# Performance work log

Hardware: AMD Instinct MI355X
Metric: run time of the kernel (lower is better)

Reference implementation:

```python
import jax, jax.numpy as jnp
import numpy as np

B, A, L, D, IN = 4096, 11, 8, 256, 4
HID = 64  # mlp_dim in MS_HGNN modules
LINE = 64  # line_embedding output dim


def setup_inputs() -> dict:
    key = jax.random.key(0)
    ks = jax.random.split(key, 17)
    s = 0.02
    f = jnp.float32
    return {
        "inputs": jax.random.normal(ks[0], (B * A, L, IN), f),
        "W_in": jax.random.normal(ks[1], (IN, D), f) * s,
        "b_in": jnp.zeros((D,), f),
        "W_pos": jax.random.normal(ks[2], (2 * D, D), f) * s,
        "b_pos": jnp.zeros((D,), f),
        "W_fc2": jax.random.normal(ks[3], (L * D, D), f) * s,
        "b_fc2": jnp.zeros((D,), f),
        "W_fc3": jax.random.normal(ks[4], (D + A, D), f) * s,
        "b_fc3": jnp.zeros((D,), f),
        "Wh1": jax.random.normal(ks[5], (D, HID), f) * s,
        "We1": jax.random.normal(ks[6], (2 * HID, HID), f) * s,
        "Wn1": jax.random.normal(ks[7], (HID, D), f) * s,
        "Wh2": jax.random.normal(ks[8], (D, HID), f) * s,
        "We2": jax.random.normal(ks[9], (2 * HID, HID), f) * s,
        "Wn2": jax.random.normal(ks[10], (HID, D), f) * s,
        "W_line": jax.random.normal(ks[11], (D, LINE), f) * s,
        "batch_size": B,
        "agent_num": A,
    }


def _nmp(xf, Wh, We, Wn, w=None):
    # one round of neural message passing over the (hyper)graph of agents
    h = jax.nn.relu(xf @ Wh)  # [B, A, HID]
    b, a, hd = h.shape
    hi = jnp.broadcast_to(h[:, :, None, :], (b, a, a, hd))
    hj = jnp.broadcast_to(h[:, None, :, :], (b, a, a, hd))
    e = jax.nn.relu(jnp.concatenate([hi, hj], -1) @ We)  # [B, A, A, HID]
    if w is None:
        agg = e.mean(axis=2)
    else:
        agg = (w[..., None] * e).sum(axis=2) / (w.sum(axis=2)[..., None] + 1e-6)
    return agg @ Wn  # [B, A, D]


def reference(inputs, W_in, b_in, W_pos, b_pos, W_fc2, b_fc2, W_fc3, b_fc3,
              Wh1, We1, Wn1, Wh2, We2, Wn2, W_line, batch_size, agent_num):
    d = W_in.shape[1]
    length = inputs.shape[1]
    # input_fc
    tf_in = inputs @ W_in + b_in  # [B*A, L, D]
    # positional encoding (sin/cos interleaved), concat + fc (dropout in eval)
    pos = jnp.arange(length, dtype=tf_in.dtype)[:, None]
    div = jnp.exp(jnp.arange(0, d, 2, dtype=tf_in.dtype) * (-np.log(10000.0) / d))
    ang = pos * div  # [L, D/2]
    pe = jnp.stack([jnp.sin(ang), jnp.cos(ang)], -1).reshape(length, d)
    x = jnp.concatenate([tf_in, jnp.broadcast_to(pe, tf_in.shape)], -1) @ W_pos + b_pos
    # flatten time, input_fc2
    x = x.reshape(batch_size, agent_num, length * d)
    ftraj = x @ W_fc2 + b_fc2  # [B, A, D]
    # add_category (identity one-hot per agent) + input_fc3
    eye = jnp.broadcast_to(jnp.eye(agent_num, dtype=ftraj.dtype),
                           (batch_size, agent_num, agent_num))
    ftraj = jnp.concatenate([ftraj, eye], -1) @ W_fc3 + b_fc3
    # cosine-similarity correlation + per-scene adaptive thresholding
    q = ftraj / jnp.linalg.norm(ftraj, axis=2, keepdims=True)
    corr = jnp.einsum('bad,bcd->bac', q, q)
    a = corr.min(axis=(1, 2), keepdims=True)
    thr = jnp.where(a < 0.4, 0.4,
                    jnp.where((a > 0.4) & (a < 0.6), a + 0.1, a + 0.03))
    corr = jnp.where(corr < thr, jnp.zeros_like(corr), corr)
    adj = (corr > 0).astype(ftraj.dtype)  # binarized dynamic grouping mask
    # ordinary fully-connected interaction
    ftraj_inter = _nmp(ftraj, Wh1, We1, Wn1)
    # group-masked hyper interaction + line embedding
    hyp = _nmp(ftraj, Wh2, We2, Wn2, adj)
    feat_one = hyp @ W_line  # [B, A, LINE]
    out = jnp.concatenate([ftraj, ftraj_inter, feat_one], -1)
    return out.reshape(batch_size * agent_num, -1)
```

## Files before the change

### kernel.cpp

```cpp
#include <hip/hip_runtime.h>

#define TPB 256

constexpr int B_ = 4096, A_ = 11;
constexpr int R_ = B_ * A_;
constexpr int K32 = 32;

constexpr int M_O     = 0;
constexpr int M2_O    = 8192;
constexpr int WC_O    = 16384;
constexpr int XBASE_O = 17408;
constexpr int PE_O    = 17664;
constexpr int XB_O    = 19712;
constexpr int CB_O    = 21760;
constexpr int B2_O    = 22016;
constexpr int WN2L_O  = 24832;
constexpr int MH1_O   = 28928;
constexpr int BH1_O   = 30976;
constexpr int MH2_O   = 16384;
constexpr int BH2_O   = 18432;
constexpr int U1_O    = 32768;
constexpr int SZ_RH   = R_ * 64;
constexpr int V1_O    = U1_O + SZ_RH;
constexpr int U2_O    = V1_O + SZ_RH;
constexpr int V2_O    = U2_O + SZ_RH;


__global__ __launch_bounds__(TPB) void k_preA(const float* __restrict__ Win,
                                              const float* __restrict__ bin,
                                              const float* __restrict__ Wpos,
                                              const float* __restrict__ bpos,
                                              float* __restrict__ ws) {
    __shared__ float red[8 * 33];
    const int t = threadIdx.x, o8 = t & 31, ks = t >> 5;
    const int bx = blockIdx.x;
    if (bx < 32) {
        int o = bx * 32 + o8, i = o >> 8, j = o & 255;
        const float* Ar = Win + i * 256;
        float p = 0.f;
        #pragma unroll 8
        for (int d = ks * 32; d < ks * 32 + 32; ++d) p += Ar[d] * Wpos[d * 256 + j];
        red[ks * 33 + o8] = p;
        __syncthreads();
        if (t < 32) {
            float s = 0.f;
            #pragma unroll
            for (int m = 0; m < 8; ++m) s += red[m * 33 + t];
            ws[WC_O + bx * 32 + t] = s;
        }
    } else if (bx < 40) {
        int j = (bx - 32) * 32 + o8;
        float p = 0.f;
        #pragma unroll 8
        for (int d = ks * 32; d < ks * 32 + 32; ++d) p += bin[d] * Wpos[d * 256 + j];
        red[ks * 33 + o8] = p;
        __syncthreads();
        if (t < 32) {
            float s = bpos[(bx - 32) * 32 + t];
            #pragma unroll
            for (int m = 0; m < 8; ++m) s += red[m * 33 + t];
            ws[XBASE_O + (bx - 32) * 32 + t] = s;
        }
    } else {
        int o = (bx - 40) * 256 + t;
        int l = o >> 8, dd = o & 255;
        const float c0 = -logf(10000.f) / 256.f;
        float freq = expf((float)(dd & ~1) * c0);
        float ang = (float)l * freq;
        ws[PE_O + o] = (dd & 1) ? cosf(ang) : sinf(ang);
    }
}

__global__ __launch_bounds__(TPB) void k_preB(const float* __restrict__ Wpos,
                                              float* __restrict__ ws) {
    __shared__ float red[8 * 33];
    const int t = threadIdx.x, o8 = t & 31, ks = t >> 5;
    int o = blockIdx.x * 32 + o8, l = o >> 8, j = o & 255;
    const float* per = ws + PE_O + l * 256;
    float p = 0.f;
    #pragma unroll 8
    for (int d = ks * 32; d < ks * 32 + 32; ++d) p += per[d] * Wpos[(256 + d) * 256 + j];
    red[ks * 33 + o8] = p;
    __syncthreads();
    if (t < 32) {
        int oo = blockIdx.x * 32 + t;
        float s = ws[XBASE_O + (oo & 255)];
        #pragma unroll
        for (int m = 0; m < 8; ++m) s += red[m * 33 + t];
        ws[XB_O + oo] = s;
    }
}

__global__ __launch_bounds__(TPB) void k_preC(const float* __restrict__ Wfc2,
                                              const float* __restrict__ bfc2,
                                              float* __restrict__ ws) {
    __shared__ float red[8 * 33];
    const int t = threadIdx.x, o8 = t & 31, ks = t >> 5;
    const int bx = blockIdx.x;
    if (bx < 256) {
        int o = bx * 32 + o8, k = o >> 8, j = o & 255;
        int l = k >> 2, i = k & 3;
        const float* Ar = ws + WC_O + i * 256;
        const float* Br = Wfc2 + l * 65536 + j;
        float p = 0.f;
        #pragma unroll 8
        for (int d = ks * 32; d < ks * 32 + 32; ++d) p += Ar[d] * Br[d * 256];
        red[ks * 33 + o8] = p;
        __syncthreads();
        if (t < 32) {
            float s = 0.f;
            #pragma unroll
            for (int m = 0; m < 8; ++m) s += red[m * 33 + t];
            ws[M_O + bx * 32 + t] = s;
        }
    } else {
        int j = (bx - 256) * 32 + o8;
        const float* Ar = ws + XB_O;
        float p = 0.f;
        #pragma unroll 4
        for (int dk = ks * 256; dk < ks * 256 + 256; ++dk) p += Ar[dk] * Wfc2[dk * 256 + j];
        red[ks * 33 + o8] = p;
        __syncthreads();
        if (t < 32) {
            int jj = (bx - 256) * 32 + t;
            float s = bfc2[jj];
            #pragma unroll
            for (int m = 0; m < 8; ++m) s += red[m * 33 + t];
            ws[CB_O + jj] = s;
        }
    }
}

__global__ __launch_bounds__(TPB) void k_preD(const float* __restrict__ Wfc3,
                                              const float* __restrict__ bfc3,
                                              const float* __restrict__ Wn2,
                                              const float* __restrict__ Wline,
                                              float* __restrict__ ws) {
    __shared__ float red[8 * 33];
    const int t = threadIdx.x, o8 = t & 31, ks = t >> 5;
    const int bx = blockIdx.x;
    if (bx < 256) {
        int o = bx * 32 + o8, k = o >> 8, j = o & 255;
        const float* Ar = ws + M_O + k * 256;
        float p = 0.f;
        #pragma unroll 8
        for (int d = ks * 32; d < ks * 32 + 32; ++d) p += Ar[d] * Wfc3[d * 256 + j];
        red[ks * 33 + o8] = p;
        __syncthreads();
        if (t < 32) {
            float s = 0.f;
            #pragma unroll
            for (int m = 0; m < 8; ++m) s += red[m * 33 + t];
            ws[M2_O + bx * 32 + t] = s;
        }
    } else if (bx < 344) {
        int o = (bx - 256) * 32 + o8, a = o >> 8, j = o & 255;
        const float* Ar = ws + CB_O;
        float p = 0.f;
        #pragma unroll 8
        for (int d = ks * 32; d < ks * 32 + 32; ++d) p += Ar[d] * Wfc3[d * 256 + j];
        red[ks * 33 + o8] = p;
        __syncthreads();
        if (t < 32) {
            int oo = (bx - 256) * 32 + t;
            int aa = oo >> 8, jj = oo & 255;
            float s = bfc3[jj] + Wfc3[(256 + aa) * 256 + jj];
            #pragma unroll
            for (int m = 0; m < 8; ++m) s += red[m * 33 + t];
            ws[B2_O + oo] = s;
        }
    } else {
        int o = (bx - 344) * 32 + o8, k = o >> 6, c = o & 63;
        const float* Ar = Wn2 + k * 256;
        float p = 0.f;
        #pragma unroll 8
        for (int d = ks * 32; d < ks * 32 + 32; ++d) p += Ar[d] * Wline[d * 64 + c];
        red[ks * 33 + o8] = p;
        __syncthreads();
        if (t < 32) {
            float s = 0.f;
            #pragma unroll
            for (int m = 0; m < 8; ++m) s += red[m * 33 + t];
            ws[WN2L_O + (bx - 344) * 32 + t] = s;
        }
    }
}

__global__ __launch_bounds__(TPB) void k_preE(const float* __restrict__ Wh1,
                                              const float* __restrict__ Wh2,
                                              float* __restrict__ ws) {
    __shared__ float red[8 * 33];
    const int t = threadIdx.x, o8 = t & 31, ks = t >> 5;
    const int bx = blockIdx.x;
    const float* Aw;  const float* Bw;  int oo_base;  int out_o;  int mode;
    if (bx < 64)       { mode = 0; out_o = MH1_O; oo_base = bx * 32;         Bw = Wh1; }
    else if (bx < 86)  { mode = 1; out_o = BH1_O; oo_base = (bx - 64) * 32;  Bw = Wh1; }
    else if (bx < 150) { mode = 0; out_o = MH2_O; oo_base = (bx - 86) * 32;  Bw = Wh2; }
    else               { mode = 1; out_o = BH2_O; oo_base = (bx - 150) * 32; Bw = Wh2; }
    int o = oo_base + o8;
    int r = o >> 6, c = o & 63;
    Aw = ws + (mode == 0 ? M2_O : B2_O) + r * 256;
    float p = 0.f;
    #pragma unroll 8
    for (int d = ks * 32; d < ks * 32 + 32; ++d) p += Aw[d] * Bw[d * 64 + c];
    red[ks * 33 + o8] = p;
    __syncthreads();
    if (t < 32) {
        float s = 0.f;
        #pragma unroll
        for (int m = 0; m < 8; ++m) s += red[m * 33 + t];
        ws[out_o + oo_base + t] = s;
    }
}


__global__ __launch_bounds__(TPB) void k_rows3(const float* __restrict__ in,
                                               const float* __restrict__ We1g,
                                               const float* __restrict__ We2g,
                                               float* __restrict__ ws,
                                               float* __restrict__ out) {
    __shared__ float inS[64 * 32];
    __shared__ float hS[64 * 64];
    __shared__ float Bs[4096];
    const int t = threadIdx.x;
    const int rowBase = blockIdx.x * 64;
    const int tg = t >> 4, tc = t & 15;
    const int r0 = tg * 4;

    {
        const float4* src = (const float4*)(in + (size_t)rowBase * K32);
        float4* dst = (float4*)inS;
        dst[t] = src[t];
        dst[t + 256] = src[t + 256];
    }
    __syncthreads();

    int ag[4];
    #pragma unroll
    for (int r = 0; r < 4; ++r) ag[r] = (rowBase + r0 + r) % 11;

    {
        float acc[4][16];
        #pragma unroll
        for (int r = 0; r < 4; ++r)
            #pragma unroll
            for (int c = 0; c < 16; ++c) acc[r][c] = 0.f;
        for (int kh = 0; kh < 2; ++kh) {
            if (kh) __syncthreads();
            {
                const float4* src = (const float4*)(ws + M2_O + kh * 4096);
                float4* dst = (float4*)Bs;
                #pragma unroll
                for (int m = 0; m < 4; ++m) dst[t + m * 256] = src[t + m * 256];
            }
            __syncthreads();
            #pragma unroll
            for (int kq = 0; kq < 4; ++kq) {
                float avq[4][4];
                #pragma unroll
                for (int r = 0; r < 4; ++r) {
                    float4 a4 = *(const float4*)&inS[(r0 + r) * 32 + kh * 16 + kq * 4];
                    avq[r][0] = a4.x; avq[r][1] = a4.y; avq[r][2] = a4.z; avq[r][3] = a4.w;
                }
                #pragma unroll
                for (int kk = 0; kk < 4; ++kk) {
                    float4 b[4];
                    #pragma unroll
                    for (int j = 0; j < 4; ++j)
                        b[j] = *(const float4*)&Bs[(kq * 4 + kk) * 256 + tc * 16 + j * 4];
                    #pragma unroll
                    for (int r = 0; r < 4; ++r) {
                        float a = avq[r][kk];
                        #pragma unroll
                        for (int j = 0; j < 4; ++j) {
                            acc[r][j * 4 + 0] += a * b[j].x;
                            acc[r][j * 4 + 1] += a * b[j].y;
                            acc[r][j * 4 + 2] += a * b[j].z;
                            acc[r][j * 4 + 3] += a * b[j].w;
                        }
                    }
                }
            }
        }
        #pragma unroll
        for (int r = 0; r < 4; ++r) {
            size_t ob = (size_t)(rowBase + r0 + r) * 576 + tc * 16;
            const float* bb = ws + B2_O + ag[r] * 256 + tc * 16;
            #pragma unroll
            for (int j = 0; j < 4; ++j) {
                float4 b = *(const float4*)&bb[j * 4];
                *(float4*)&out[ob + j * 4] =
                    make_float4(acc[r][j * 4 + 0] + b.x, acc[r][j * 4 + 1] + b.y,
                                acc[r][j * 4 + 2] + b.z, acc[r][j * 4 + 3] + b.w);
            }
        }
    }

    const int c0 = tc * 4;
    for (int s = 0; s < 2; ++s) {
        const int mh_o = s ? MH2_O : MH1_O;
        const int bh_o = s ? BH2_O : BH1_O;
        const float* We = s ? We2g : We1g;
        float* ug = ws + (s ? U2_O : U1_O);
        float* vg = ws + (s ? V2_O : V1_O);

        __syncthreads();
        {
            const float4* src = (const float4*)(ws + mh_o);
            float4* dst = (float4*)Bs;
            dst[t] = src[t];
            if (t < 256) dst[t + 256] = src[t + 256];
        }
        __syncthreads();
        float hacc[4][4];
        #pragma unroll
        for (int r = 0; r < 4; ++r)
            #pragma unroll
            for (int c = 0; c < 4; ++c) hacc[r][c] = 0.f;
        #pragma unroll
        for (int kq = 0; kq < 8; ++kq) {
            float avq[4][4];
            #pragma unroll
            for (int r = 0; r < 4; ++r) {
                float4 a4 = *(const float4*)&inS[(r0 + r) * 32 + kq * 4];
                avq[r][0] = a4.x; avq[r][1] = a4.y; avq[r][2] = a4.z; avq[r][3] = a4.w;
            }
            #pragma unroll
            for (int kk = 0; kk < 4; ++kk) {
                float4 b = *(const float4*)&Bs[(kq * 4 + kk) * 64 + c0];
                #pragma unroll
                for (int r = 0; r < 4; ++r) {
                    float a = avq[r][kk];
                    hacc[r][0] += a * b.x; hacc[r][1] += a * b.y;
                    hacc[r][2] += a * b.z; hacc[r][3] += a * b.w;
                }
            }
        }
        #pragma unroll
        for (int r = 0; r < 4; ++r) {
            float4 b = *(const float4*)&ws[bh_o + ag[r] * 64 + c0];
            float4 h = make_float4(fmaxf(hacc[r][0] + b.x, 0.f), fmaxf(hacc[r][1] + b.y, 0.f),
                                   fmaxf(hacc[r][2] + b.z, 0.f), fmaxf(hacc[r][3] + b.w, 0.f));
            *(float4*)&hS[(r0 + r) * 64 + c0] = h;
        }
        __syncthreads();

        float ua[4][4], va[4][4];
        #pragma unroll
        for (int r = 0; r < 4; ++r)
            #pragma unroll
            for (int c = 0; c < 4; ++c) { ua[r][c] = 0.f; va[r][c] = 0.f; }
        for (int kh = 0; kh < 2; ++kh) {
            if (kh) __syncthreads();
            {
                const float4* s0 = (const float4*)(We + kh * 2048);
                const float4* s1 = (const float4*)(We + 4096 + kh * 2048);
                float4* dst = (float4*)Bs;
                dst[t] = s0[t];
                if (t < 256) dst[t + 256] = s0[t + 256];
                dst[t + 512] = s1[t];
                if (t < 256) dst[t + 768] = s1[t + 256];
            }
            __syncthreads();
            #pragma unroll
            for (int kq = 0; kq < 8; ++kq) {
                float avq[4][4];
                #pragma unroll
                for (int r = 0; r < 4; ++r) {
                    float4 a4 = *(const float4*)&hS[(r0 + r) * 64 + kh * 32 + kq * 4];
                    avq[r][0] = a4.x; avq[r][1] = a4.y; avq[r][2] = a4.z; avq[r][3] = a4.w;
                }
                #pragma unroll
                for (int kk = 0; kk < 4; ++kk) {
                    float4 bu = *(const float4*)&Bs[(kq * 4 + kk) * 64 + c0];
                    float4 bv = *(const float4*)&Bs[2048 + (kq * 4 + kk) * 64 + c0];
                    #pragma unroll
                    for (int r = 0; r < 4; ++r) {
                        float a = avq[r][kk];
                        ua[r][0] += a * bu.x; ua[r][1] += a * bu.y;
                        ua[r][2] += a * bu.z; ua[r][3] += a * bu.w;
                        va[r][0] += a * bv.x; va[r][1] += a * bv.y;
                        va[r][2] += a * bv.z; va[r][3] += a * bv.w;
                    }
                }
            }
        }
        #pragma unroll
        for (int r = 0; r < 4; ++r) {
            size_t rb = (size_t)(rowBase + r0 + r) * 64 + c0;
            *(float4*)&ug[rb] = make_float4(ua[r][0], ua[r][1], ua[r][2], ua[r][3]);
            *(float4*)&vg[rb] = make_float4(va[r][0], va[r][1], va[r][2], va[r][3]);
        }
    }
}


__global__ __launch_bounds__(TPB) void k_scene3(const float* __restrict__ out_ft,
                                                const float* __restrict__ Wn1,
                                                float* __restrict__ ws,
                                                float* __restrict__ out) {
    __shared__ float ftS[11 * 260];
    __shared__ float u1s[704], v1s[704], u2s[704], v2s[704];
    __shared__ float dots[121];
    __shared__ float corrv[121];
    __shared__ float red[4];
    __shared__ float sthr;
    const int t = threadIdx.x;
    const int scene = blockIdx.x;
    const int base = scene * 11;

    for (int o = t; o < 704; o += TPB) {
        int row = o >> 6, c4 = o & 63;
        ((float4*)ftS)[row * 65 + c4] =
            *(const float4*)&out_ft[(size_t)(base + row) * 576 + c4 * 4];
    }
    {
        const float4* su1 = (const float4*)(ws + U1_O + (size_t)base * 64);
        const float4* sv1 = (const float4*)(ws + V1_O + (size_t)base * 64);
        const float4* su2 = (const float4*)(ws + U2_O + (size_t)base * 64);
        const float4* sv2 = (const float4*)(ws + V2_O + (size_t)base * 64);
        if (t < 176) {
            ((float4*)u1s)[t] = su1[t];
            ((float4*)v1s)[t] = sv1[t];
            ((float4*)u2s)[t] = su2[t];
            ((float4*)v2s)[t] = sv2[t];
        }
    }
    __syncthreads();

    if (t < 121) {
        int i = t / 11, j = t - i * 11;
        float s = 0.f;
        #pragma unroll 8
        for (int kq = 0; kq < 64; ++kq) {
            float4 a = *(const float4*)&ftS[i * 260 + kq * 4];
            float4 b = *(const float4*)&ftS[j * 260 + kq * 4];
            s += a.x * b.x + a.y * b.y + a.z * b.z + a.w * b.w;
        }
        dots[t] = s;
    }
    __syncthreads();
    if (t < 121) {
        int i = t / 11, j = t - i * 11;
        corrv[t] = dots[t] * rsqrtf(dots[i * 11 + i] * dots[j * 11 + j]);
    }
    __syncthreads();
    float v = (t < 121) ? corrv[t] : 3.0e38f;
    for (int off = 32; off > 0; off >>= 1) v = fminf(v, __shfl_down(v, off));
    if ((t & 63) == 0) red[t >> 6] = v;
    __syncthreads();
    if (t == 0) {
        float a = fminf(fminf(red[0], red[1]), fminf(red[2], red[3]));
        sthr = (a < 0.4f) ? 0.4f : ((a > 0.4f && a < 0.6f) ? a + 0.1f : a + 0.03f);
    }
    __syncthreads();
    const float thr = sthr;

    {
        const int c = t & 63, g = t >> 6;
        const int nr = (g == 3) ? 2 : 3;
        float u1[3], u2[3], s1[3], s2[3], cnt[3];
        #pragma unroll
        for (int r = 0; r < 3; ++r) { s1[r] = 0.f; s2[r] = 0.f; cnt[r] = 0.f; }
        for (int r = 0; r < nr; ++r) {
            u1[r] = u1s[(g + 4 * r) * 64 + c];
            u2[r] = u2s[(g + 4 * r) * 64 + c];
        }
        #pragma unroll
        for (int j = 0; j < 11; ++j) {
            float vv1 = v1s[j * 64 + c];
            float vv2 = v2s[j * 64 + c];
            for (int r = 0; r < nr; ++r) {
                float cw = corrv[(g + 4 * r) * 11 + j];
                s1[r] += fmaxf(u1[r] + vv1, 0.f);
                float adj = (cw >= thr) ? 1.f : 0.f;
                s2[r] += adj * fmaxf(u2[r] + vv2, 0.f);
                cnt[r] += adj;
            }
        }
        for (int r = 0; r < nr; ++r) {
            u1s[(g + 4 * r) * 64 + c] = s1[r] * (1.f / 11.f);
            u2s[(g + 4 * r) * 64 + c] = s2[r] / (cnt[r] + 1e-6f);
        }
    }
    __syncthreads();

    {
        const int c = t;
        float breg[64];
        #pragma unroll
        for (int k = 0; k < 64; ++k) breg[k] = Wn1[k * 256 + c];
        float acc[11];
        #pragma unroll
        for (int i = 0; i < 11; ++i) acc[i] = 0.f;
        #pragma unroll
        for (int kq = 0; kq < 16; ++kq) {
            #pragma unroll
            for (int i = 0; i < 11; ++i) {
                float4 a = *(const float4*)&u1s[i * 64 + kq * 4];
                acc[i] += a.x * breg[kq * 4 + 0] + a.y * breg[kq * 4 + 1]
                        + a.z * breg[kq * 4 + 2] + a.w * breg[kq * 4 + 3];
            }
        }
        #pragma unroll
        for (int i = 0; i < 11; ++i)
            out[(size_t)(base + i) * 576 + 256 + c] = acc[i];
    }
    {
        const int c = t & 63, g = t >> 6;
        const int nr = (g == 3) ? 2 : 3;
        float wreg[64];
        #pragma unroll
        for (int k = 0; k < 64; ++k) wreg[k] = ws[WN2L_O + k * 64 + c];
        float acc[3] = {0.f, 0.f, 0.f};
        #pragma unroll
        for (int kq = 0; kq < 16; ++kq) {
            for (int r = 0; r < nr; ++r) {
                float4 a = *(const float4*)&u2s[(g + 4 * r) * 64 + kq * 4];
                acc[r] += a.x * wreg[kq * 4 + 0] + a.y * wreg[kq * 4 + 1]
                        + a.z * wreg[kq * 4 + 2] + a.w * wreg[kq * 4 + 3];
            }
        }
        for (int r = 0; r < nr; ++r)
            out[(size_t)(base + g + 4 * r) * 576 + 512 + c] = acc[r];
    }
}

extern "C" void kernel_launch(void* const* d_in, const int* in_sizes, int n_in,
                              void* d_out, int out_size, void* d_ws, size_t ws_size,
                              hipStream_t stream) {
    (void)in_sizes; (void)n_in; (void)out_size; (void)ws_size;
    const float* in     = (const float*)d_in[0];
    const float* W_in   = (const float*)d_in[1];
    const float* b_in   = (const float*)d_in[2];
    const float* W_pos  = (const float*)d_in[3];
    const float* b_pos  = (const float*)d_in[4];
    const float* W_fc2  = (const float*)d_in[5];
    const float* b_fc2  = (const float*)d_in[6];
    const float* W_fc3  = (const float*)d_in[7];
    const float* b_fc3  = (const float*)d_in[8];
    const float* Wh1    = (const float*)d_in[9];
    const float* We1    = (const float*)d_in[10];
    const float* Wn1    = (const float*)d_in[11];
    const float* Wh2    = (const float*)d_in[12];
    const float* We2    = (const float*)d_in[13];
    const float* Wn2    = (const float*)d_in[14];
    const float* W_line = (const float*)d_in[15];
    float* out = (float*)d_out;
    float* ws  = (float*)d_ws;

    k_preA<<<48, TPB, 0, stream>>>(W_in, b_in, W_pos, b_pos, ws);
    k_preB<<<64, TPB, 0, stream>>>(W_pos, ws);
    k_preC<<<264, TPB, 0, stream>>>(W_fc2, b_fc2, ws);
    k_preD<<<472, TPB, 0, stream>>>(W_fc3, b_fc3, Wn2, W_line, ws);
    k_preE<<<172, TPB, 0, stream>>>(Wh1, Wh2, ws);
    k_rows3<<<R_ / 64, TPB, 0, stream>>>(in, We1, We2, ws, out);
    k_scene3<<<B_, TPB, 0, stream>>>(out, Wn1, ws, out);
}
```

Measured before the change: 177.6 us.

## Fuse per-row projection and per-scene message passing into one kernel

Replaces the separate row kernel (which wrote u/v intermediates to workspace) and the scene kernel (which reread ftraj and u/v) with a single kernel. Each 64-lane wave handles one whole scene and computes ftraj, the correlation threshold, both message-passing rounds and the output projections on-chip. The positional-encoding precompute is also merged into one setup kernel, and the Wn2·W_line product moves there, cutting one launch. This removes the large intermediate global round-trips and a launch. The cost is heavy register use (11-row accumulators) and many block barriers in the fused kernel.

```diff
diff --git a/kernel.cpp b/kernel.cpp
--- a/kernel.cpp
+++ b/kernel.cpp
@@ -4,13 +4,10 @@
 
 constexpr int B_ = 4096, A_ = 11;
 constexpr int R_ = B_ * A_;
-constexpr int K32 = 32;
 
 constexpr int M_O     = 0;
 constexpr int M2_O    = 8192;
 constexpr int WC_O    = 16384;
-constexpr int XBASE_O = 17408;
-constexpr int PE_O    = 17664;
 constexpr int XB_O    = 19712;
 constexpr int CB_O    = 21760;
 constexpr int B2_O    = 22016;
@@ -19,18 +16,15 @@
 constexpr int BH1_O   = 30976;
 constexpr int MH2_O   = 16384;
 constexpr int BH2_O   = 18432;
-constexpr int U1_O    = 32768;
-constexpr int SZ_RH   = R_ * 64;
-constexpr int V1_O    = U1_O + SZ_RH;
-constexpr int U2_O    = V1_O + SZ_RH;
-constexpr int V2_O    = U2_O + SZ_RH;
-
-
-__global__ __launch_bounds__(TPB) void k_preA(const float* __restrict__ Win,
-                                              const float* __restrict__ bin,
-                                              const float* __restrict__ Wpos,
-                                              const float* __restrict__ bpos,
-                                              float* __restrict__ ws) {
+
+
+__global__ __launch_bounds__(TPB) void k_preAB(const float* __restrict__ Win,
+                                               const float* __restrict__ bin,
+                                               const float* __restrict__ Wpos,
+                                               const float* __restrict__ bpos,
+                                               const float* __restrict__ Wn2,
+                                               const float* __restrict__ Wline,
+                                               float* __restrict__ ws) {
     __shared__ float red[8 * 33];
     const int t = threadIdx.x, o8 = t & 31, ks = t >> 5;
     const int bx = blockIdx.x;
@@ -48,46 +42,44 @@
             for (int m = 0; m < 8; ++m) s += red[m * 33 + t];
             ws[WC_O + bx * 32 + t] = s;
         }
-    } else if (bx < 40) {
-        int j = (bx - 32) * 32 + o8;
+    } else if (bx < 96) {
+        int o = (bx - 32) * 32 + o8, l = o >> 8, j = o & 255;
+        const float c0 = -logf(10000.f) / 256.f;
+        float p = 0.f;
+        for (int d = ks * 64; d < ks * 64 + 64; ++d) {
+            float a;
+            if (d < 256) a = bin[d];
+            else {
+                int dd = d - 256;
+                float freq = expf((float)(dd & ~1) * c0);
+                float ang = (float)l * freq;
+                a = (dd & 1) ? cosf(ang) : sinf(ang);
+            }
+            p += a * Wpos[d * 256 + j];
+        }
+        red[ks * 33 + o8] = p;
+        __syncthreads();
+        if (t < 32) {
+            int oo = (bx - 32) * 32 + t;
+            float s = bpos[oo & 255];
+            #pragma unroll
+            for (int m = 0; m < 8; ++m) s += red[m * 33 + t];
+            ws[XB_O + oo] = s;
+        }
+    } else {
+        int o = (bx - 96) * 32 + o8, k = o >> 6, c = o & 63;
+        const float* Ar = Wn2 + k * 256;
         float p = 0.f;
         #pragma unroll 8
-        for (int d = ks * 32; d < ks * 32 + 32; ++d) p += bin[d] * Wpos[d * 256 + j];
-        red[ks * 33 + o8] = p;
-        __syncthreads();
-        if (t < 32) {
-            float s = bpos[(bx - 32) * 32 + t];
-            #pragma unroll
-            for (int m = 0; m < 8; ++m) s += red[m * 33 + t];
-            ws[XBASE_O + (bx - 32) * 32 + t] = s;
-        }
-    } else {
-        int o = (bx - 40) * 256 + t;
-        int l = o >> 8, dd = o & 255;
-        const float c0 = -logf(10000.f) / 256.f;
-        float freq = expf((float)(dd & ~1) * c0);
-        float ang = (float)l * freq;
-        ws[PE_O + o] = (dd & 1) ? cosf(ang) : sinf(ang);
-    }
-}
-
-__global__ __launch_bounds__(TPB) void k_preB(const float* __restrict__ Wpos,
-                                              float* __restrict__ ws) {
-    __shared__ float red[8 * 33];
-    const int t = threadIdx.x, o8 = t & 31, ks = t >> 5;
-    int o = blockIdx.x * 32 + o8, l = o >> 8, j = o & 255;
-    const float* per = ws + PE_O + l * 256;
-    float p = 0.f;
-    #pragma unroll 8
-    for (int d = ks * 32; d < ks * 32 + 32; ++d) p += per[d] * Wpos[(256 + d) * 256 + j];
-    red[ks * 33 + o8] = p;
-    __syncthreads();
-    if (t < 32) {
-        int oo = blockIdx.x * 32 + t;
-        float s = ws[XBASE_O + (oo & 255)];
-        #pragma unroll
-        for (int m = 0; m < 8; ++m) s += red[m * 33 + t];
-        ws[XB_O + oo] = s;
+        for (int d = ks * 32; d < ks * 32 + 32; ++d) p += Ar[d] * Wline[d * 64 + c];
+        red[ks * 33 + o8] = p;
+        __syncthreads();
+        if (t < 32) {
+            float s = 0.f;
+            #pragma unroll
+            for (int m = 0; m < 8; ++m) s += red[m * 33 + t];
+            ws[WN2L_O + (bx - 96) * 32 + t] = s;
+        }
     }
 }
 
@@ -133,8 +125,6 @@
 
 __global__ __launch_bounds__(TPB) void k_preD(const float* __restrict__ Wfc3,
                                               const float* __restrict__ bfc3,
-                                              const float* __restrict__ Wn2,
-                                              const float* __restrict__ Wline,
                                               float* __restrict__ ws) {
     __shared__ float red[8 * 33];
     const int t = threadIdx.x, o8 = t & 31, ks = t >> 5;
@@ -153,8 +143,8 @@
             for (int m = 0; m < 8; ++m) s += red[m * 33 + t];
             ws[M2_O + bx * 32 + t] = s;
         }
-    } else if (bx < 344) {
-        int o = (bx - 256) * 32 + o8, a = o >> 8, j = o & 255;
+    } else {
+        int o = (bx - 256) * 32 + o8, j = o & 255;
         const float* Ar = ws + CB_O;
         float p = 0.f;
         #pragma unroll 8
@@ -168,20 +158,6 @@
             #pragma unroll
             for (int m = 0; m < 8; ++m) s += red[m * 33 + t];
             ws[B2_O + oo] = s;
-        }
-    } else {
-        int o = (bx - 344) * 32 + o8, k = o >> 6, c = o & 63;
-        const float* Ar = Wn2 + k * 256;
-        float p = 0.f;
-        #pragma unroll 8
-        for (int d = ks * 32; d < ks * 32 + 32; ++d) p += Ar[d] * Wline[d * 64 + c];
-        red[ks * 33 + o8] = p;
-        __syncthreads();
-        if (t < 32) {
-            float s = 0.f;
-            #pragma unroll
-            for (int m = 0; m < 8; ++m) s += red[m * 33 + t];
-            ws[WN2L_O + (bx - 344) * 32 + t] = s;
         }
     }
 }
@@ -192,14 +168,14 @@
     __shared__ float red[8 * 33];
     const int t = threadIdx.x, o8 = t & 31, ks = t >> 5;
     const int bx = blockIdx.x;
-    const float* Aw;  const float* Bw;  int oo_base;  int out_o;  int mode;
+    const float* Bw;  int oo_base;  int out_o;  int mode;
     if (bx < 64)       { mode = 0; out_o = MH1_O; oo_base = bx * 32;         Bw = Wh1; }
     else if (bx < 86)  { mode = 1; out_o = BH1_O; oo_base = (bx - 64) * 32;  Bw = Wh1; }
     else if (bx < 150) { mode = 0; out_o = MH2_O; oo_base = (bx - 86) * 32;  Bw = Wh2; }
     else               { mode = 1; out_o = BH2_O; oo_base = (bx - 150) * 32; Bw = Wh2; }
     int o = oo_base + o8;
     int r = o >> 6, c = o & 63;
-    Aw = ws + (mode == 0 ? M2_O : B2_O) + r * 256;
+    const float* Aw = ws + (mode == 0 ? M2_O : B2_O) + r * 256;
     float p = 0.f;
     #pragma unroll 8
     for (int d = ks * 32; d < ks * 32 + 32; ++d) p += Aw[d] * Bw[d * 64 + c];
@@ -214,315 +190,262 @@
 }
 
 
-__global__ __launch_bounds__(TPB) void k_rows3(const float* __restrict__ in,
-                                               const float* __restrict__ We1g,
-                                               const float* __restrict__ We2g,
-                                               float* __restrict__ ws,
-                                               float* __restrict__ out) {
-    __shared__ float inS[64 * 32];
-    __shared__ float hS[64 * 64];
-    __shared__ float Bs[4096];
+__device__ __forceinline__ void fma4(float4& a, float s, const float4& b) {
+    a.x += s * b.x; a.y += s * b.y; a.z += s * b.z; a.w += s * b.w;
+}
+
+__global__ __launch_bounds__(TPB, 4) void k_fused(const float* __restrict__ in,
+                                                  const float* __restrict__ We1g,
+                                                  const float* __restrict__ We2g,
+                                                  const float* __restrict__ Wn1,
+                                                  const float* __restrict__ ws,
+                                                  float* __restrict__ out) {
+    __shared__ float inS[44 * 36];
+    __shared__ float cS[44 * 68];
+    __shared__ float Bs[2048];
+    __shared__ float dotsS[4 * 121];
+    __shared__ float corrS[4 * 121];
     const int t = threadIdx.x;
-    const int rowBase = blockIdx.x * 64;
-    const int tg = t >> 4, tc = t & 15;
-    const int r0 = tg * 4;
-
+    const int w = t >> 6, lane = t & 63;
+    const int rowBlk = blockIdx.x * 44;
+    const int wr = w * 11;
+
+    for (int o = t; o < 352; o += TPB) {
+        int row = o >> 3, c4 = o & 7;
+        *(float4*)&inS[row * 36 + c4 * 4] =
+            *(const float4*)&in[(size_t)(rowBlk + row) * 32 + c4 * 4];
+    }
+
+    int pi0 = 0, pj0 = 0, pi1 = 0, pj1 = 0;
+    const bool has0 = lane < 66;
+    const bool has1 = lane < 2;
     {
-        const float4* src = (const float4*)(in + (size_t)rowBase * K32);
-        float4* dst = (float4*)inS;
-        dst[t] = src[t];
-        dst[t + 256] = src[t + 256];
-    }
-    __syncthreads();
-
-    int ag[4];
+        int q = has0 ? lane : 0, i = 0;
+        while (q >= 11 - i) { q -= 11 - i; ++i; }
+        pi0 = i; pj0 = i + q;
+        if (has1) {
+            int q2 = lane + 64, i2 = 0;
+            while (q2 >= 11 - i2) { q2 -= 11 - i2; ++i2; }
+            pi1 = i2; pj1 = i2 + q2;
+        }
+    }
+    __syncthreads();
+
+    float4 ft[11];
+    {
+        const float* M2g = ws + M2_O;
+        #pragma unroll
+        for (int i = 0; i < 11; ++i) ft[i] = make_float4(0.f, 0.f, 0.f, 0.f);
+        #pragma unroll
+        for (int kq = 0; kq < 8; ++kq) {
+            float4 b[4];
+            #pragma unroll
+            for (int kk = 0; kk < 4; ++kk)
+                b[kk] = *(const float4*)&M2g[(kq * 4 + kk) * 256 + lane * 4];
+            #pragma unroll
+            for (int i = 0; i < 11; ++i) {
+                float4 a4 = *(const float4*)&inS[(wr + i) * 36 + kq * 4];
+                fma4(ft[i], a4.x, b[0]); fma4(ft[i], a4.y, b[1]);
+                fma4(ft[i], a4.z, b[2]); fma4(ft[i], a4.w, b[3]);
+            }
+        }
+        #pragma unroll
+        for (int i = 0; i < 11; ++i) {
+            float4 b2 = *(const float4*)&ws[B2_O + i * 256 + lane * 4];
+            ft[i].x += b2.x; ft[i].y += b2.y; ft[i].z += b2.z; ft[i].w += b2.w;
+            *(float4*)&out[(size_t)(rowBlk + wr + i) * 576 + lane * 4] = ft[i];
+        }
+    }
+
+    float dacc0 = 0.f, dacc1 = 0.f;
+    for (int ch = 0; ch < 4; ++ch) {
+        __syncthreads();
+        if ((lane >> 4) == ch) {
+            int cl = (lane & 15) * 4;
+            #pragma unroll
+            for (int i = 0; i < 11; ++i)
+                *(float4*)&cS[(wr + i) * 68 + cl] = ft[i];
+        }
+        __syncthreads();
+        if (has0) {
+            const float* ra = &cS[(wr + pi0) * 68];
+            const float* rb = &cS[(wr + pj0) * 68];
+            #pragma unroll
+            for (int cc = 0; cc < 16; ++cc) {
+                float4 a = *(const float4*)&ra[cc * 4];
+                float4 b = *(const float4*)&rb[cc * 4];
+                dacc0 += a.x * b.x + a.y * b.y + a.z * b.z + a.w * b.w;
+            }
+        }
+        if (has1) {
+            const float* ra = &cS[(wr + pi1) * 68];
+            const float* rb = &cS[(wr + pj1) * 68];
+            #pragma unroll
+            for (int cc = 0; cc < 16; ++cc) {
+                float4 a = *(const float4*)&ra[cc * 4];
+                float4 b = *(const float4*)&rb[cc * 4];
+                dacc1 += a.x * b.x + a.y * b.y + a.z * b.z + a.w * b.w;
+            }
+        }
+    }
+    if (has0) { dotsS[w * 121 + pi0 * 11 + pj0] = dacc0;
+                dotsS[w * 121 + pj0 * 11 + pi0] = dacc0; }
+    if (has1) { dotsS[w * 121 + pi1 * 11 + pj1] = dacc1;
+                dotsS[w * 121 + pj1 * 11 + pi1] = dacc1; }
+    __syncthreads();
+
+    float thr;
+    {
+        const float* dw = &dotsS[w * 121];
+        int q = lane, i = q / 11, j = q % 11;
+        float c0 = dw[q] * rsqrtf(dw[i * 11 + i] * dw[j * 11 + j]);
+        corrS[w * 121 + q] = c0;
+        float mn = c0;
+        int q2 = lane + 64;
+        if (q2 < 121) {
+            int i2 = q2 / 11, j2 = q2 % 11;
+            float c1 = dw[q2] * rsqrtf(dw[i2 * 11 + i2] * dw[j2 * 11 + j2]);
+            corrS[w * 121 + q2] = c1;
+            mn = fminf(mn, c1);
+        }
+        #pragma unroll
+        for (int off = 32; off; off >>= 1) mn = fminf(mn, __shfl_xor(mn, off));
+        thr = (mn < 0.4f) ? 0.4f : ((mn > 0.4f && mn < 0.6f) ? mn + 0.1f : mn + 0.03f);
+    }
+
+    float agg1[11], agg2[11];
+    for (int st = 0; st < 2; ++st) {
+        const float* Weg = st ? We2g : We1g;
+        const float* bhg = ws + (st ? BH2_O : BH1_O);
+        __syncthreads();
+        {
+            const float4* src = (const float4*)(ws + (st ? MH2_O : MH1_O));
+            ((float4*)Bs)[t] = src[t];
+            ((float4*)Bs)[t + 256] = src[t + 256];
+        }
+        __syncthreads();
+        float h[11];
+        {
+            #pragma unroll
+            for (int i = 0; i < 11; ++i) h[i] = 0.f;
+            #pragma unroll
+            for (int kq = 0; kq < 8; ++kq) {
+                float bq[4];
+                #pragma unroll
+                for (int kk = 0; kk < 4; ++kk) bq[kk] = Bs[(kq * 4 + kk) * 64 + lane];
+                #pragma unroll
+                for (int i = 0; i < 11; ++i) {
+                    float4 a4 = *(const float4*)&inS[(wr + i) * 36 + kq * 4];
+                    h[i] += a4.x * bq[0] + a4.y * bq[1] + a4.z * bq[2] + a4.w * bq[3];
+                }
+            }
+            #pragma unroll
+            for (int i = 0; i < 11; ++i)
+                h[i] = fmaxf(h[i] + bhg[i * 64 + lane], 0.f);
+        }
+        __syncthreads();
+        #pragma unroll
+        for (int i = 0; i < 11; ++i) cS[(wr + i) * 68 + lane] = h[i];
+
+        float u[11], v[11];
+        #pragma unroll
+        for (int i = 0; i < 11; ++i) { u[i] = 0.f; v[i] = 0.f; }
+        for (int kh = 0; kh < 4; ++kh) {
+            __syncthreads();
+            {
+                int k = t >> 4, c4 = t & 15;
+                ((float4*)Bs)[t] = *(const float4*)&Weg[(kh * 16 + k) * 64 + c4 * 4];
+                ((float4*)(Bs + 1024))[t] = *(const float4*)&Weg[(64 + kh * 16 + k) * 64 + c4 * 4];
+            }
+            __syncthreads();
+            #pragma unroll
+            for (int kq = 0; kq < 4; ++kq) {
+                float bu[4], bv[4];
+                #pragma unroll
+                for (int kk = 0; kk < 4; ++kk) {
+                    bu[kk] = Bs[(kq * 4 + kk) * 64 + lane];
+                    bv[kk] = Bs[1024 + (kq * 4 + kk) * 64 + lane];
+                }
+                #pragma unroll
+                for (int i = 0; i < 11; ++i) {
+                    float4 a4 = *(const float4*)&cS[(wr + i) * 68 + kh * 16 + kq * 4];
+                    u[i] += a4.x * bu[0] + a4.y * bu[1] + a4.z * bu[2] + a4.w * bu[3];
+                    v[i] += a4.x * bv[0] + a4.y * bv[1] + a4.z * bv[2] + a4.w * bv[3];
+                }
+            }
+        }
+        if (st == 0) {
+            #pragma unroll
+            for (int i = 0; i < 11; ++i) {
+                float s = 0.f;
+                #pragma unroll
+                for (int j = 0; j < 11; ++j) s += fmaxf(u[i] + v[j], 0.f);
+                agg1[i] = s * (1.f / 11.f);
+            }
+        } else {
+            #pragma unroll
+            for (int i = 0; i < 11; ++i) {
+                float s = 0.f, cnt = 0.f;
+                #pragma unroll
+                for (int j = 0; j < 11; ++j) {
+                    float adj = (corrS[w * 121 + i * 11 + j] >= thr) ? 1.f : 0.f;
+                    s += adj * fmaxf(u[i] + v[j], 0.f);
+                    cnt += adj;
+                }
+                agg2[i] = s / (cnt + 1e-6f);
+            }
+        }
+    }
+
+    __syncthreads();
     #pragma unroll
-    for (int r = 0; r < 4; ++r) ag[r] = (rowBase + r0 + r) % 11;
-
+    for (int i = 0; i < 11; ++i) cS[(wr + i) * 68 + lane] = agg1[i];
+    __syncthreads();
     {
-        float acc[4][16];
-        #pragma unroll
-        for (int r = 0; r < 4; ++r)
-            #pragma unroll
-            for (int c = 0; c < 16; ++c) acc[r][c] = 0.f;
-        for (int kh = 0; kh < 2; ++kh) {
-            if (kh) __syncthreads();
-            {
-                const float4* src = (const float4*)(ws + M2_O + kh * 4096);
-                float4* dst = (float4*)Bs;
-                #pragma unroll
-                for (int m = 0; m < 4; ++m) dst[t + m * 256] = src[t + m * 256];
-            }
-            __syncthreads();
-            #pragma unroll
-            for (int kq = 0; kq < 4; ++kq) {
-                float avq[4][4];
-                #pragma unroll
-                for (int r = 0; r < 4; ++r) {
-                    float4 a4 = *(const float4*)&inS[(r0 + r) * 32 + kh * 16 + kq * 4];
-                    avq[r][0] = a4.x; avq[r][1] = a4.y; avq[r][2] = a4.z; avq[r][3] = a4.w;
-                }
-                #pragma unroll
-                for (int kk = 0; kk < 4; ++kk) {
-                    float4 b[4];
-                    #pragma unroll
-                    for (int j = 0; j < 4; ++j)
-                        b[j] = *(const float4*)&Bs[(kq * 4 + kk) * 256 + tc * 16 + j * 4];
-                    #pragma unroll
-                    for (int r = 0; r < 4; ++r) {
-                        float a = avq[r][kk];
-                        #pragma unroll
-                        for (int j = 0; j < 4; ++j) {
-                            acc[r][j * 4 + 0] += a * b[j].x;
-                            acc[r][j * 4 + 1] += a * b[j].y;
-                            acc[r][j * 4 + 2] += a * b[j].z;
-                            acc[r][j * 4 + 3] += a * b[j].w;
-                        }
-                    }
-                }
-            }
-        }
-        #pragma unroll
-        for (int r = 0; r < 4; ++r) {
-            size_t ob = (size_t)(rowBase + r0 + r) * 576 + tc * 16;
-            const float* bb = ws + B2_O + ag[r] * 256 + tc * 16;
-            #pragma unroll
-            for (int j = 0; j < 4; ++j) {
-                float4 b = *(const float4*)&bb[j * 4];
-                *(float4*)&out[ob + j * 4] =
-                    make_float4(acc[r][j * 4 + 0] + b.x, acc[r][j * 4 + 1] + b.y,
-                                acc[r][j * 4 + 2] + b.z, acc[r][j * 4 + 3] + b.w);
-            }
-        }
-    }
-
-    const int c0 = tc * 4;
-    for (int s = 0; s < 2; ++s) {
-        const int mh_o = s ? MH2_O : MH1_O;
-        const int bh_o = s ? BH2_O : BH1_O;
-        const float* We = s ? We2g : We1g;
-        float* ug = ws + (s ? U2_O : U1_O);
-        float* vg = ws + (s ? V2_O : V1_O);
-
-        __syncthreads();
-        {
-            const float4* src = (const float4*)(ws + mh_o);
-            float4* dst = (float4*)Bs;
-            dst[t] = src[t];
-            if (t < 256) dst[t + 256] = src[t + 256];
-        }
-        __syncthreads();
-        float hacc[4][4];
-        #pragma unroll
-        for (int r = 0; r < 4; ++r)
-            #pragma unroll
-            for (int c = 0; c < 4; ++c) hacc[r][c] = 0.f;
-        #pragma unroll
-        for (int kq = 0; kq < 8; ++kq) {
-            float avq[4][4];
-            #pragma unroll
-            for (int r = 0; r < 4; ++r) {
-                float4 a4 = *(const float4*)&inS[(r0 + r) * 32 + kq * 4];
-                avq[r][0] = a4.x; avq[r][1] = a4.y; avq[r][2] = a4.z; avq[r][3] = a4.w;
-            }
-            #pragma unroll
-            for (int kk = 0; kk < 4; ++kk) {
-                float4 b = *(const float4*)&Bs[(kq * 4 + kk) * 64 + c0];
-                #pragma unroll
-                for (int r = 0; r < 4; ++r) {
-                    float a = avq[r][kk];
-                    hacc[r][0] += a * b.x; hacc[r][1] += a * b.y;
-                    hacc[r][2] += a * b.z; hacc[r][3] += a * b.w;
-                }
-            }
-        }
-        #pragma unroll
-        for (int r = 0; r < 4; ++r) {
-            float4 b = *(const float4*)&ws[bh_o + ag[r] * 64 + c0];
-            float4 h = make_float4(fmaxf(hacc[r][0] + b.x, 0.f), fmaxf(hacc[r][1] + b.y, 0.f),
-                                   fmaxf(hacc[r][2] + b.z, 0.f), fmaxf(hacc[r][3] + b.w, 0.f));
-            *(float4*)&hS[(r0 + r) * 64 + c0] = h;
-        }
-        __syncthreads();
-
-        float ua[4][4], va[4][4];
-        #pragma unroll
-        for (int r = 0; r < 4; ++r)
-            #pragma unroll
-            for (int c = 0; c < 4; ++c) { ua[r][c] = 0.f; va[r][c] = 0.f; }
-        for (int kh = 0; kh < 2; ++kh) {
-            if (kh) __syncthreads();
-            {
-                const float4* s0 = (const float4*)(We + kh * 2048);
-                const float4* s1 = (const float4*)(We + 4096 + kh * 2048);
-                float4* dst = (float4*)Bs;
-                dst[t] = s0[t];
-                if (t < 256) dst[t + 256] = s0[t + 256];
-                dst[t + 512] = s1[t];
-                if (t < 256) dst[t + 768] = s1[t + 256];
-            }
-            __syncthreads();
-            #pragma unroll
-            for (int kq = 0; kq < 8; ++kq) {
-                float avq[4][4];
-                #pragma unroll
-                for (int r = 0; r < 4; ++r) {
-                    float4 a4 = *(const float4*)&hS[(r0 + r) * 64 + kh * 32 + kq * 4];
-                    avq[r][0] = a4.x; avq[r][1] = a4.y; avq[r][2] = a4.z; avq[r][3] = a4.w;
-                }
-                #pragma unroll
-                for (int kk = 0; kk < 4; ++kk) {
-                    float4 bu = *(const float4*)&Bs[(kq * 4 + kk) * 64 + c0];
-                    float4 bv = *(const float4*)&Bs[2048 + (kq * 4 + kk) * 64 + c0];
-                    #pragma unroll
-                    for (int r = 0; r < 4; ++r) {
-                        float a = avq[r][kk];
-                        ua[r][0] += a * bu.x; ua[r][1] += a * bu.y;
-                        ua[r][2] += a * bu.z; ua[r][3] += a * bu.w;
-                        va[r][0] += a * bv.x; va[r][1] += a * bv.y;
-                        va[r][2] += a * bv.z; va[r][3] += a * bv.w;
-                    }
-                }
-            }
-        }
-        #pragma unroll
-        for (int r = 0; r < 4; ++r) {
-            size_t rb = (size_t)(rowBase + r0 + r) * 64 + c0;
-            *(float4*)&ug[rb] = make_float4(ua[r][0], ua[r][1], ua[r][2], ua[r][3]);
-            *(float4*)&vg[rb] = make_float4(va[r][0], va[r][1], va[r][2], va[r][3]);
-        }
-    }
-}
-
-
-__global__ __launch_bounds__(TPB) void k_scene3(const float* __restrict__ out_ft,
-                                                const float* __restrict__ Wn1,
-                                                float* __restrict__ ws,
-                                                float* __restrict__ out) {
-    __shared__ float ftS[11 * 260];
-    __shared__ float u1s[704], v1s[704], u2s[704], v2s[704];
-    __shared__ float dots[121];
-    __shared__ float corrv[121];
-    __shared__ float red[4];
-    __shared__ float sthr;
-    const int t = threadIdx.x;
-    const int scene = blockIdx.x;
-    const int base = scene * 11;
-
-    for (int o = t; o < 704; o += TPB) {
-        int row = o >> 6, c4 = o & 63;
-        ((float4*)ftS)[row * 65 + c4] =
-            *(const float4*)&out_ft[(size_t)(base + row) * 576 + c4 * 4];
-    }
+        float4 acc[11];
+        #pragma unroll
+        for (int i = 0; i < 11; ++i) acc[i] = make_float4(0.f, 0.f, 0.f, 0.f);
+        #pragma unroll 4
+        for (int kq = 0; kq < 16; ++kq) {
+            float4 b[4];
+            #pragma unroll
+            for (int kk = 0; kk < 4; ++kk)
+                b[kk] = *(const float4*)&Wn1[(kq * 4 + kk) * 256 + lane * 4];
+            #pragma unroll
+            for (int i = 0; i < 11; ++i) {
+                float4 a4 = *(const float4*)&cS[(wr + i) * 68 + kq * 4];
+                fma4(acc[i], a4.x, b[0]); fma4(acc[i], a4.y, b[1]);
+                fma4(acc[i], a4.z, b[2]); fma4(acc[i], a4.w, b[3]);
+            }
+        }
+        #pragma unroll
+        for (int i = 0; i < 11; ++i)
+            *(float4*)&out[(size_t)(rowBlk + wr + i) * 576 + 256 + lane * 4] = acc[i];
+    }
+
+    __syncthreads();
+    #pragma unroll
+    for (int i = 0; i < 11; ++i) cS[(wr + i) * 68 + lane] = agg2[i];
+    __syncthreads();
     {
-        const float4* su1 = (const float4*)(ws + U1_O + (size_t)base * 64);
-        const float4* sv1 = (const float4*)(ws + V1_O + (size_t)base * 64);
-        const float4* su2 = (const float4*)(ws + U2_O + (size_t)base * 64);
-        const float4* sv2 = (const float4*)(ws + V2_O + (size_t)base * 64);
-        if (t < 176) {
-            ((float4*)u1s)[t] = su1[t];
-            ((float4*)v1s)[t] = sv1[t];
-            ((float4*)u2s)[t] = su2[t];
-            ((float4*)v2s)[t] = sv2[t];
-        }
-    }
-    __syncthreads();
-
-    if (t < 121) {
-        int i = t / 11, j = t - i * 11;
-        float s = 0.f;
-        #pragma unroll 8
-        for (int kq = 0; kq < 64; ++kq) {
-            float4 a = *(const float4*)&ftS[i * 260 + kq * 4];
-            float4 b = *(const float4*)&ftS[j * 260 + kq * 4];
-            s += a.x * b.x + a.y * b.y + a.z * b.z + a.w * b.w;
-        }
-        dots[t] = s;
-    }
-    __syncthreads();
-    if (t < 121) {
-        int i = t / 11, j = t - i * 11;
-        corrv[t] = dots[t] * rsqrtf(dots[i * 11 + i] * dots[j * 11 + j]);
-    }
-    __syncthreads();
-    float v = (t < 121) ? corrv[t] : 3.0e38f;
-    for (int off = 32; off > 0; off >>= 1) v = fminf(v, __shfl_down(v, off));
-    if ((t & 63) == 0) red[t >> 6] = v;
-    __syncthreads();
-    if (t == 0) {
-        float a = fminf(fminf(red[0], red[1]), fminf(red[2], red[3]));
-        sthr = (a < 0.4f) ? 0.4f : ((a > 0.4f && a < 0.6f) ? a + 0.1f : a + 0.03f);
-    }
-    __syncthreads();
-    const float thr = sthr;
-
-    {
-        const int c = t & 63, g = t >> 6;
-        const int nr = (g == 3) ? 2 : 3;
-        float u1[3], u2[3], s1[3], s2[3], cnt[3];
-        #pragma unroll
-        for (int r = 0; r < 3; ++r) { s1[r] = 0.f; s2[r] = 0.f; cnt[r] = 0.f; }
-        for (int r = 0; r < nr; ++r) {
-            u1[r] = u1s[(g + 4 * r) * 64 + c];
-            u2[r] = u2s[(g + 4 * r) * 64 + c];
-        }
-        #pragma unroll
-        for (int j = 0; j < 11; ++j) {
-            float vv1 = v1s[j * 64 + c];
-            float vv2 = v2s[j * 64 + c];
-            for (int r = 0; r < nr; ++r) {
-                float cw = corrv[(g + 4 * r) * 11 + j];
-                s1[r] += fmaxf(u1[r] + vv1, 0.f);
-                float adj = (cw >= thr) ? 1.f : 0.f;
-                s2[r] += adj * fmaxf(u2[r] + vv2, 0.f);
-                cnt[r] += adj;
-            }
-        }
-        for (int r = 0; r < nr; ++r) {
-            u1s[(g + 4 * r) * 64 + c] = s1[r] * (1.f / 11.f);
-            u2s[(g + 4 * r) * 64 + c] = s2[r] / (cnt[r] + 1e-6f);
-        }
-    }
-    __syncthreads();
-
-    {
-        const int c = t;
-        float breg[64];
-        #pragma unroll
-        for (int k = 0; k < 64; ++k) breg[k] = Wn1[k * 256 + c];
-        float acc[11];
-        #pragma unroll
-        for (int i = 0; i < 11; ++i) acc[i] = 0.f;
-        #pragma unroll
+        float f[11];
+        #pragma unroll
+        for (int i = 0; i < 11; ++i) f[i] = 0.f;
+        const float* W2 = ws + WN2L_O;
+        #pragma unroll 4
         for (int kq = 0; kq < 16; ++kq) {
+            float bq[4];
+            #pragma unroll
+            for (int kk = 0; kk < 4; ++kk) bq[kk] = W2[(kq * 4 + kk) * 64 + lane];
             #pragma unroll
             for (int i = 0; i < 11; ++i) {
-                float4 a = *(const float4*)&u1s[i * 64 + kq * 4];
-                acc[i] += a.x * breg[kq * 4 + 0] + a.y * breg[kq * 4 + 1]
-                        + a.z * breg[kq * 4 + 2] + a.w * breg[kq * 4 + 3];
+                float4 a4 = *(const float4*)&cS[(wr + i) * 68 + kq * 4];
+                f[i] += a4.x * bq[0] + a4.y * bq[1] + a4.z * bq[2] + a4.w * bq[3];
             }
         }
         #pragma unroll
         for (int i = 0; i < 11; ++i)
-            out[(size_t)(base + i) * 576 + 256 + c] = acc[i];
-    }
-    {
-        const int c = t & 63, g = t >> 6;
-        const int nr = (g == 3) ? 2 : 3;
-        float wreg[64];
-        #pragma unroll
-        for (int k = 0; k < 64; ++k) wreg[k] = ws[WN2L_O + k * 64 + c];
-        float acc[3] = {0.f, 0.f, 0.f};
-        #pragma unroll
-        for (int kq = 0; kq < 16; ++kq) {
-            for (int r = 0; r < nr; ++r) {
-                float4 a = *(const float4*)&u2s[(g + 4 * r) * 64 + kq * 4];
-                acc[r] += a.x * wreg[kq * 4 + 0] + a.y * wreg[kq * 4 + 1]
-                        + a.z * wreg[kq * 4 + 2] + a.w * wreg[kq * 4 + 3];
-            }
-        }
-        for (int r = 0; r < nr; ++r)
-            out[(size_t)(base + g + 4 * r) * 576 + 512 + c] = acc[r];
+            out[(size_t)(rowBlk + wr + i) * 576 + 512 + lane] = f[i];
     }
 }
 
@@ -549,11 +472,9 @@
     float* out = (float*)d_out;
     float* ws  = (float*)d_ws;
 
-    k_preA<<<48, TPB, 0, stream>>>(W_in, b_in, W_pos, b_pos, ws);
-    k_preB<<<64, TPB, 0, stream>>>(W_pos, ws);
+    k_preAB<<<224, TPB, 0, stream>>>(W_in, b_in, W_pos, b_pos, Wn2, W_line, ws);
     k_preC<<<264, TPB, 0, stream>>>(W_fc2, b_fc2, ws);
-    k_preD<<<472, TPB, 0, stream>>>(W_fc3, b_fc3, Wn2, W_line, ws);
+    k_preD<<<344, TPB, 0, stream>>>(W_fc3, b_fc3, ws);
     k_preE<<<172, TPB, 0, stream>>>(Wh1, Wh2, ws);
-    k_rows3<<<R_ / 64, TPB, 0, stream>>>(in, We1, We2, ws, out);
-    k_scene3<<<B_, TPB, 0, stream>>>(out, Wn1, ws, out);
-}
+    k_fused<<<B_ / 4, TPB, 0, stream>>>(in, We1, We2, Wn1, ws, out);
+}
```

After: 313.3 us. 76.4% more time.
